# Kernel optimization log

Measured on AMD Instinct MI355X. Metric: run time of the kernel, lower is better.

Reference implementation:

```python
import jax, jax.numpy as jnp
import numpy as np

B, T, D, H, W = 256, 512, 64, 128, 256

def _init_linear(key, out_dim, in_dim):
    lim = 1.0 / np.sqrt(in_dim)
    return jax.random.uniform(key, (out_dim, in_dim), jnp.float32, -lim, lim)

def setup_inputs():
    key = jax.random.key(0)
    ks = jax.random.split(key, 12)
    inp = {}
    inp['ts'] = jnp.arange(T, dtype=jnp.float32)
    for n, k in zip(['coeffs_d', 'coeffs_c', 'coeffs_b', 'coeffs_a'], ks[:4]):
        inp[n] = jax.random.normal(k, (B, T - 1, D), jnp.float32) * 0.05
    # initial MLP: D -> W -> W -> H (relu hidden, identity final)
    inp['i_w0'] = _init_linear(ks[4], W, D); inp['i_b0'] = jnp.zeros((W,), jnp.float32)
    inp['i_w1'] = _init_linear(ks[5], W, W); inp['i_b1'] = jnp.zeros((W,), jnp.float32)
    inp['i_w2'] = _init_linear(ks[6], H, W); inp['i_b2'] = jnp.zeros((H,), jnp.float32)
    # func MLP: H -> W -> W -> H*D (softplus hidden, tanh final)
    inp['f_w0'] = _init_linear(ks[7], W, H); inp['f_b0'] = jnp.zeros((W,), jnp.float32)
    inp['f_w1'] = _init_linear(ks[8], W, W); inp['f_b1'] = jnp.zeros((W,), jnp.float32)
    inp['f_w2'] = _init_linear(ks[9], H * D, W); inp['f_b2'] = jnp.zeros((H * D,), jnp.float32)
    # readout linear: H -> 1
    inp['l_w'] = _init_linear(ks[10], 1, H); inp['l_b'] = jnp.zeros((1,), jnp.float32)
    return inp

def reference(ts, coeffs_d, coeffs_c, coeffs_b, coeffs_a,
              i_w0, i_b0, i_w1, i_b1, i_w2, i_b2,
              f_w0, f_b0, f_w1, f_b1, f_w2, f_b2,
              l_w, l_b):
    dt = ts[1] - ts[0]
    # cubic spline value at t=ts[0]: interval 0, frac 0 -> a[0]
    x0 = coeffs_a[:, 0, :]  # [B, D]
    h = jax.nn.relu(x0 @ i_w0.T + i_b0)
    h = jax.nn.relu(h @ i_w1.T + i_b1)
    y0 = h @ i_w2.T + i_b2  # [B, H]

    def step(carry, _):
        t, y = carry
        # cubic spline derivative at t: b + 2c*frac + 3d*frac^2 on interval idx
        idx = jnp.clip(jnp.searchsorted(ts, t, side='right') - 1, 0, T - 2)
        frac = t - ts[idx]
        deriv = coeffs_b[:, idx] + 2.0 * coeffs_c[:, idx] * frac + 3.0 * coeffs_d[:, idx] * (frac * frac)  # [B, D]
        # vector field f(y): [B, H, D]
        g = jax.nn.softplus(y @ f_w0.T + f_b0)
        g = jax.nn.softplus(g @ f_w1.T + f_b1)
        f = jnp.tanh(g @ f_w2.T + f_b2).reshape(B, H, D)
        # Euler step: y1 = y + (f @ dX/dt) * dt
        y1 = y + jnp.einsum('bhd,bd->bh', f, deriv) * dt
        return (t + dt, y1), y1

    _, ys = jax.lax.scan(step, (ts[0], y0), None, length=T)
    # prediction = sigmoid(linear(ys[-1]))[0], per batch element
    return jax.nn.sigmoid(ys[-1] @ l_w.T + l_b)[:, 0]  # [B]
```

## Files before the change

### kernel.cpp

```cpp
#include <hip/hip_runtime.h>
#include <hip/hip_bf16.h>
#include <stdint.h>


#define BB 256
#define DD 64
#define HH 128
#define WW 256
#define HD 8192
#define TSTEPS 512
#define PAD_Y 152
#define PAD_G 280

typedef __bf16 bf16x8 __attribute__((ext_vector_type(8)));
typedef __bf16 bf16x4 __attribute__((ext_vector_type(4)));
typedef float f32x4 __attribute__((ext_vector_type(4)));

__device__ __forceinline__ float softplus_f(float x) {
  return (x > 15.f) ? x : __logf(1.f + __expf(x));
}
__device__ __forceinline__ float tanh_f(float x) {
  float e = __expf(2.f * x);
  return 1.f - 2.f / (e + 1.f);
}
__device__ __forceinline__ float aloadf(const float* p) {
  return __hip_atomic_load(p, __ATOMIC_RELAXED, __HIP_MEMORY_SCOPE_AGENT);
}
__device__ __forceinline__ void astoref(float* p, float v) {
  __hip_atomic_store(p, v, __ATOMIC_RELAXED, __HIP_MEMORY_SCOPE_AGENT);
}
__device__ __forceinline__ uint32_t aloadu(const uint32_t* p) {
  return __hip_atomic_load(p, __ATOMIC_RELAXED, __HIP_MEMORY_SCOPE_AGENT);
}
__device__ __forceinline__ void astoreu(uint32_t* p, uint32_t v) {
  __hip_atomic_store(p, v, __ATOMIC_RELAXED, __HIP_MEMORY_SCOPE_AGENT);
}

__global__ void prep_kernel(const float* __restrict__ w0, const float* __restrict__ w1,
                            const float* __restrict__ w2,
                            __bf16* __restrict__ w0b, __bf16* __restrict__ w1b,
                            __bf16* __restrict__ w2b) {
  int stride = gridDim.x * blockDim.x;
  int i0 = blockIdx.x * blockDim.x + threadIdx.x;
  for (int i = i0; i < WW * HH; i += stride) w0b[i] = (__bf16)w0[i];
  for (int i = i0; i < WW * WW; i += stride) w1b[i] = (__bf16)w1[i];
  for (int i = i0; i < HD * WW; i += stride) w2b[i] = (__bf16)w2[i];
}

__global__ __launch_bounds__(256) void init_kernel(
    const float* __restrict__ ca, const float* __restrict__ iw0, const float* __restrict__ ib0,
    const float* __restrict__ iw1, const float* __restrict__ ib1,
    const float* __restrict__ iw2, const float* __restrict__ ib2,
    float* __restrict__ y0) {
  __shared__ float x0[DD];
  __shared__ float h0[WW];
  __shared__ float h1[WW];
  int b = blockIdx.x, t = threadIdx.x;
  if (t < DD) x0[t] = ca[((size_t)b * 511) * DD + t];
  __syncthreads();
  float a = ib0[t];
  for (int d = 0; d < DD; ++d) a = fmaf(x0[d], iw0[t * DD + d], a);
  h0[t] = fmaxf(a, 0.f);
  __syncthreads();
  a = ib1[t];
  for (int d = 0; d < WW; ++d) a = fmaf(h0[d], iw1[t * WW + d], a);
  h1[t] = fmaxf(a, 0.f);
  __syncthreads();
  if (t < HH) {
    a = ib2[t];
    for (int d = 0; d < WW; ++d) a = fmaf(h1[d], iw2[t * WW + d], a);
    y0[b * HH + t] = a;
  }
}

__global__ __launch_bounds__(512, 2) void step_persist(
    const __bf16* __restrict__ w0b, const __bf16* __restrict__ w1b, const __bf16* __restrict__ w2b,
    const float* __restrict__ fb0, const float* __restrict__ fb1, const float* __restrict__ fb2,
    const float* __restrict__ cbp, const float* __restrict__ ccp, const float* __restrict__ cdp,
    float* __restrict__ yA, float* __restrict__ pk, uint32_t* __restrict__ yflag)
{
  __shared__ __align__(16) __bf16 w2l[32768];
  __shared__ __align__(16) __bf16 yb[32 * PAD_Y];
  __shared__ __align__(16) __bf16 g0s[32 * PAD_G];
  __shared__ __align__(16) __bf16 g1s[32 * PAD_G];
  __shared__ float pbuf[8 * 32];

  const int tid = threadIdx.x;
  const int wv = tid >> 6;
  const int l = tid & 63;
  const int l16 = l & 15;
  const int lq = l >> 4;

  const int wid = blockIdx.x;
  const int grp = wid >> 5;
  const int j = wid & 31;
  const int rb = grp * 32;
  const int c0 = j * 256;

  for (int it = 0; it < 8; ++it) {
    int blk = tid + it * 512;
    int kq = blk >> 7, cl = blk & 127;
    int wv2 = cl >> 4, l16b = cl & 15;
    int kb = kq >> 2, lq2 = kq & 3;
    int col = c0 + wv2 * 32 + l16b;
    *(bf16x8*)&w2l[blk * 8] =
        *(const bf16x8*)&w2b[(size_t)col * WW + kb * 32 + lq2 * 8];
  }
  const int w2base = lq * 1024 + wv * 128 + l16 * 8;

  bf16x8 w0f[4][2], w1f[8][2], w2f1[8];
  #pragma unroll
  for (int c = 0; c < 2; ++c) {
    int col = wv * 32 + c * 16 + l16;
    #pragma unroll
    for (int kb = 0; kb < 4; ++kb)
      w0f[kb][c] = *(const bf16x8*)&w0b[col * HH + kb * 32 + lq * 8];
    #pragma unroll
    for (int kb = 0; kb < 8; ++kb)
      w1f[kb][c] = *(const bf16x8*)&w1b[col * WW + kb * 32 + lq * 8];
  }
  {
    int col = c0 + wv * 32 + 16 + l16;
    #pragma unroll
    for (int kb = 0; kb < 8; ++kb)
      w2f1[kb] = *(const bf16x8*)&w2b[(size_t)col * WW + kb * 32 + lq * 8];
  }
  f32x4 b0r[2], b1r[2], b2r[2];
  #pragma unroll
  for (int c = 0; c < 2; ++c) {
    b0r[c] = *(const f32x4*)&fb0[wv * 32 + c * 16 + lq * 4];
    b1r[c] = *(const f32x4*)&fb1[wv * 32 + c * 16 + lq * 4];
    b2r[c] = *(const f32x4*)&fb2[c0 + wv * 32 + c * 16 + lq * 4];
  }

  size_t cb2[2];
  #pragma unroll
  for (int bt = 0; bt < 2; ++bt)
    cb2[bt] = ((size_t)(rb + bt * 16 + l16) * 511) * DD + (wv & 1) * 32 + lq * 4;

  float yreg = 0.f;
  int myidx = 0;
  if (tid < 128) {
    int r = tid & 31, hl = tid >> 5;
    myidx = (rb + r) * HH + (4 * j + hl);
    yreg = yA[myidx];
    astoref(&pk[myidx], yreg);
  }
  __syncthreads();
  if (tid == 0) astoreu(&yflag[grp * 32 + j], 1u);

  const int ps = tid & 31;
  const int pw = tid >> 5;
  const uint32_t* myflag = &yflag[grp * 32 + ps];

  for (int k = 0; k < TSTEPS; ++k) {
    const uint32_t want = (uint32_t)(k + 1);
    const float* src = pk + (size_t)(k & 1) * (BB * HH);
    float* dst = pk + (size_t)((k + 1) & 1) * (BB * HH);

    f32x4 dvv[2][2];
    {
      size_t ko = (size_t)((k <= 510) ? k : 510) * DD;
      #pragma unroll
      for (int bt = 0; bt < 2; ++bt)
        #pragma unroll
        for (int c = 0; c < 2; ++c) {
          size_t off = cb2[bt] + ko + c * 16;
          dvv[bt][c] = *(const f32x4*)&cbp[off];
          if (k == 511) {
            f32x4 cc = *(const f32x4*)&ccp[off];
            f32x4 dd = *(const f32x4*)&cdp[off];
            #pragma unroll
            for (int r = 0; r < 4; ++r)
              dvv[bt][c][r] += 2.f * cc[r] + 3.f * dd[r];
          }
        }
    }

    {
      int spins = 0;
      while (aloadu(myflag) < want) {
        __builtin_amdgcn_s_sleep(1);
        if (++spins > (1 << 20)) break;
      }
      __asm__ __volatile__("" ::: "memory");
      #pragma unroll
      for (int r2 = 0; r2 < 2; ++r2) {
        int row = 2 * pw + r2;
        const float* ysrc = &src[(rb + row) * HH + 4 * ps];
        bf16x4 o;
        #pragma unroll
        for (int q = 0; q < 4; ++q) o[q] = (__bf16)aloadf(&ysrc[q]);
        *(bf16x4*)&yb[row * PAD_Y + 4 * ps] = o;
      }
    }
    __syncthreads();

    {
      f32x4 acc[2][2];
      #pragma unroll
      for (int c = 0; c < 2; ++c) { acc[c][0] = b0r[c]; acc[c][1] = b0r[c]; }
      #pragma unroll
      for (int kb = 0; kb < 4; ++kb) {
        bf16x8 y0 = *(const bf16x8*)&yb[l16 * PAD_Y + kb * 32 + lq * 8];
        bf16x8 y1 = *(const bf16x8*)&yb[(16 + l16) * PAD_Y + kb * 32 + lq * 8];
        #pragma unroll
        for (int c = 0; c < 2; ++c) {
          acc[c][0] = __builtin_amdgcn_mfma_f32_16x16x32_bf16(w0f[kb][c], y0, acc[c][0], 0, 0, 0);
          acc[c][1] = __builtin_amdgcn_mfma_f32_16x16x32_bf16(w0f[kb][c], y1, acc[c][1], 0, 0, 0);
        }
      }
      #pragma unroll
      for (int c = 0; c < 2; ++c)
        #pragma unroll
        for (int bt = 0; bt < 2; ++bt) {
          bf16x4 o;
          #pragma unroll
          for (int r = 0; r < 4; ++r)
            o[r] = (__bf16)softplus_f(acc[c][bt][r]);
          *(bf16x4*)&g0s[(bt * 16 + l16) * PAD_G + wv * 32 + c * 16 + lq * 4] = o;
        }
    }
    __syncthreads();

    {
      f32x4 acc[2][2];
      #pragma unroll
      for (int c = 0; c < 2; ++c) { acc[c][0] = b1r[c]; acc[c][1] = b1r[c]; }
      #pragma unroll
      for (int kb = 0; kb < 8; ++kb) {
        bf16x8 a0 = *(const bf16x8*)&g0s[l16 * PAD_G + kb * 32 + lq * 8];
        bf16x8 a1 = *(const bf16x8*)&g0s[(16 + l16) * PAD_G + kb * 32 + lq * 8];
        #pragma unroll
        for (int c = 0; c < 2; ++c) {
          acc[c][0] = __builtin_amdgcn_mfma_f32_16x16x32_bf16(w1f[kb][c], a0, acc[c][0], 0, 0, 0);
          acc[c][1] = __builtin_amdgcn_mfma_f32_16x16x32_bf16(w1f[kb][c], a1, acc[c][1], 0, 0, 0);
        }
      }
      #pragma unroll
      for (int c = 0; c < 2; ++c)
        #pragma unroll
        for (int bt = 0; bt < 2; ++bt) {
          bf16x4 o;
          #pragma unroll
          for (int r = 0; r < 4; ++r)
            o[r] = (__bf16)softplus_f(acc[c][bt][r]);
          *(bf16x4*)&g1s[(bt * 16 + l16) * PAD_G + wv * 32 + c * 16 + lq * 4] = o;
        }
    }
    __syncthreads();

    {
      f32x4 acc[2][2];
      #pragma unroll
      for (int c = 0; c < 2; ++c) { acc[c][0] = b2r[c]; acc[c][1] = b2r[c]; }
      #pragma unroll
      for (int kb = 0; kb < 8; ++kb) {
        bf16x8 a0 = *(const bf16x8*)&g1s[l16 * PAD_G + kb * 32 + lq * 8];
        bf16x8 a1 = *(const bf16x8*)&g1s[(16 + l16) * PAD_G + kb * 32 + lq * 8];
        bf16x8 wf0 = *(const bf16x8*)&w2l[w2base + kb * 4096];
        acc[0][0] = __builtin_amdgcn_mfma_f32_16x16x32_bf16(wf0, a0, acc[0][0], 0, 0, 0);
        acc[0][1] = __builtin_amdgcn_mfma_f32_16x16x32_bf16(wf0, a1, acc[0][1], 0, 0, 0);
        acc[1][0] = __builtin_amdgcn_mfma_f32_16x16x32_bf16(w2f1[kb], a0, acc[1][0], 0, 0, 0);
        acc[1][1] = __builtin_amdgcn_mfma_f32_16x16x32_bf16(w2f1[kb], a1, acc[1][1], 0, 0, 0);
      }
      #pragma unroll
      for (int bt = 0; bt < 2; ++bt) {
        float p = 0.f;
        #pragma unroll
        for (int c = 0; c < 2; ++c) {
          #pragma unroll
          for (int r = 0; r < 4; ++r) {
            float f = tanh_f(acc[c][bt][r]);
            p = fmaf(f, dvv[bt][c][r], p);
          }
        }
        p += __shfl_xor(p, 16);
        p += __shfl_xor(p, 32);
        if (l < 16) pbuf[wv * 32 + bt * 16 + l] = p;
      }
    }
    __syncthreads();

    if (tid < 128) {
      int hl = tid >> 5, r = tid & 31;
      yreg += pbuf[(2 * hl) * 32 + r] + pbuf[(2 * hl + 1) * 32 + r];
      astoref(&dst[myidx], yreg);
    }
    __syncthreads();
    if (tid == 0) astoreu(&yflag[grp * 32 + j], (uint32_t)(k + 2));
  }

  if (tid < 128) yA[myidx] = yreg;
}

__global__ __launch_bounds__(256) void final_kernel(const float* __restrict__ y,
                                                    const float* __restrict__ lw,
                                                    const float* __restrict__ lb,
                                                    float* __restrict__ out) {
  int b = threadIdx.x;
  float a = lb[0];
  for (int h = 0; h < HH; ++h) a = fmaf(y[b * HH + h], lw[h], a);
  out[b] = 1.f / (1.f + __expf(-a));
}

extern "C" void kernel_launch(void* const* d_in, const int* in_sizes, int n_in,
                              void* d_out, int out_size, void* d_ws, size_t ws_size,
                              hipStream_t stream) {
  const float* cdp = (const float*)d_in[1];
  const float* ccp = (const float*)d_in[2];
  const float* cbp = (const float*)d_in[3];
  const float* cap = (const float*)d_in[4];
  const float* iw0 = (const float*)d_in[5];
  const float* ib0 = (const float*)d_in[6];
  const float* iw1 = (const float*)d_in[7];
  const float* ib1 = (const float*)d_in[8];
  const float* iw2 = (const float*)d_in[9];
  const float* ib2 = (const float*)d_in[10];
  const float* fw0 = (const float*)d_in[11];
  const float* fb0 = (const float*)d_in[12];
  const float* fw1 = (const float*)d_in[13];
  const float* fb1 = (const float*)d_in[14];
  const float* fw2 = (const float*)d_in[15];
  const float* fb2 = (const float*)d_in[16];
  const float* lw  = (const float*)d_in[17];
  const float* lb  = (const float*)d_in[18];

  char* ws = (char*)d_ws;
  __bf16* w0b = (__bf16*)(ws);
  __bf16* w1b = (__bf16*)(ws + 65536);
  __bf16* w2b = (__bf16*)(ws + 196608);
  float* yA = (float*)(ws + 4390912);
  float* pk = (float*)(ws + 4521984);
  uint32_t* yflag = (uint32_t*)(ws + 4784128);

  hipMemsetAsync(yflag, 0, 1024, stream);
  prep_kernel<<<512, 256, 0, stream>>>(fw0, fw1, fw2, w0b, w1b, w2b);
  init_kernel<<<BB, 256, 0, stream>>>(cap, iw0, ib0, iw1, ib1, iw2, ib2, yA);
  step_persist<<<256, 512, 0, stream>>>(w0b, w1b, w2b, fb0, fb1, fb2,
                                        cbp, ccp, cdp, yA, pk, yflag);
  final_kernel<<<1, 256, 0, stream>>>(yA, lw, lb, (float*)d_out);

  (void)in_sizes; (void)n_in; (void)out_size; (void)ws_size;
}
```

Baseline: 3.681 ms.

## Remap W2 stage so each wave owns whole h outputs, signal per-wave

The third GEMM stage now assigns each wave 16 batch rows by 64 output columns (one full h index across D), so the D-reduction finishes inside a wave via shuffles. This removes the LDS partial-sum buffer and two block-wide barriers per step. Each wave publishes its y slice and increments the group flag with an atomic add, and consumers wait for eight increments. The cost is more weight registers per wave and that correctness now rests on the vmcnt wait ordering the y stores ahead of the relaxed flag increment.

```diff
diff --git a/kernel.cpp b/kernel.cpp
--- a/kernel.cpp
+++ b/kernel.cpp
@@ -31,9 +31,6 @@
 }
 __device__ __forceinline__ uint32_t aloadu(const uint32_t* p) {
   return __hip_atomic_load(p, __ATOMIC_RELAXED, __HIP_MEMORY_SCOPE_AGENT);
-}
-__device__ __forceinline__ void astoreu(uint32_t* p, uint32_t v) {
-  __hip_atomic_store(p, v, __ATOMIC_RELAXED, __HIP_MEMORY_SCOPE_AGENT);
 }
 
 __global__ void prep_kernel(const float* __restrict__ w0, const float* __restrict__ w1,
@@ -83,7 +80,6 @@
   __shared__ __align__(16) __bf16 yb[32 * PAD_Y];
   __shared__ __align__(16) __bf16 g0s[32 * PAD_G];
   __shared__ __align__(16) __bf16 g1s[32 * PAD_G];
-  __shared__ float pbuf[8 * 32];
 
   const int tid = threadIdx.x;
   const int wv = tid >> 6;
@@ -96,19 +92,20 @@
   const int j = wid & 31;
   const int rb = grp * 32;
   const int c0 = j * 256;
+  const int rt = wv >> 2;
+  const int hq = wv & 3;
 
   for (int it = 0; it < 8; ++it) {
     int blk = tid + it * 512;
     int kq = blk >> 7, cl = blk & 127;
-    int wv2 = cl >> 4, l16b = cl & 15;
     int kb = kq >> 2, lq2 = kq & 3;
-    int col = c0 + wv2 * 32 + l16b;
+    int col = c0 + (cl >> 5) * 64 + (cl & 31);
     *(bf16x8*)&w2l[blk * 8] =
         *(const bf16x8*)&w2b[(size_t)col * WW + kb * 32 + lq2 * 8];
   }
-  const int w2base = lq * 1024 + wv * 128 + l16 * 8;
-
-  bf16x8 w0f[4][2], w1f[8][2], w2f1[8];
+  const int w2base = lq * 1024 + (hq * 32 + l16) * 8;
+
+  bf16x8 w0f[4][2], w1f[8][2], w2f[8][2];
   #pragma unroll
   for (int c = 0; c < 2; ++c) {
     int col = wv * 32 + c * 16 + l16;
@@ -118,63 +115,56 @@
     #pragma unroll
     for (int kb = 0; kb < 8; ++kb)
       w1f[kb][c] = *(const bf16x8*)&w1b[col * WW + kb * 32 + lq * 8];
-  }
-  {
-    int col = c0 + wv * 32 + 16 + l16;
+    int colC = c0 + hq * 64 + 32 + c * 16 + l16;
     #pragma unroll
     for (int kb = 0; kb < 8; ++kb)
-      w2f1[kb] = *(const bf16x8*)&w2b[(size_t)col * WW + kb * 32 + lq * 8];
-  }
-  f32x4 b0r[2], b1r[2], b2r[2];
+      w2f[kb][c] = *(const bf16x8*)&w2b[(size_t)colC * WW + kb * 32 + lq * 8];
+  }
+  f32x4 b0r[2], b1r[2], b2r[4];
   #pragma unroll
   for (int c = 0; c < 2; ++c) {
     b0r[c] = *(const f32x4*)&fb0[wv * 32 + c * 16 + lq * 4];
     b1r[c] = *(const f32x4*)&fb1[wv * 32 + c * 16 + lq * 4];
-    b2r[c] = *(const f32x4*)&fb2[c0 + wv * 32 + c * 16 + lq * 4];
-  }
-
-  size_t cb2[2];
+  }
   #pragma unroll
-  for (int bt = 0; bt < 2; ++bt)
-    cb2[bt] = ((size_t)(rb + bt * 16 + l16) * 511) * DD + (wv & 1) * 32 + lq * 4;
-
+  for (int c = 0; c < 4; ++c)
+    b2r[c] = *(const f32x4*)&fb2[c0 + hq * 64 + c * 16 + lq * 4];
+
+  const size_t dvbase = ((size_t)(rb + rt * 16 + l16) * 511) * DD + lq * 4;
+
+  const int myidx = (rb + rt * 16 + l16) * HH + (4 * j + hq);
+  uint32_t* const flg = &yflag[grp * 32 + j];
   float yreg = 0.f;
-  int myidx = 0;
-  if (tid < 128) {
-    int r = tid & 31, hl = tid >> 5;
-    myidx = (rb + r) * HH + (4 * j + hl);
+  if (l < 16) {
     yreg = yA[myidx];
     astoref(&pk[myidx], yreg);
   }
-  __syncthreads();
-  if (tid == 0) astoreu(&yflag[grp * 32 + j], 1u);
+  __asm__ __volatile__("s_waitcnt vmcnt(0)" ::: "memory");
+  if (l == 0) __hip_atomic_fetch_add(flg, 1u, __ATOMIC_RELAXED, __HIP_MEMORY_SCOPE_AGENT);
 
   const int ps = tid & 31;
   const int pw = tid >> 5;
   const uint32_t* myflag = &yflag[grp * 32 + ps];
 
   for (int k = 0; k < TSTEPS; ++k) {
-    const uint32_t want = (uint32_t)(k + 1);
+    const uint32_t want = 8u * (uint32_t)(k + 1);
     const float* src = pk + (size_t)(k & 1) * (BB * HH);
     float* dst = pk + (size_t)((k + 1) & 1) * (BB * HH);
 
-    f32x4 dvv[2][2];
-    {
-      size_t ko = (size_t)((k <= 510) ? k : 510) * DD;
-      #pragma unroll
-      for (int bt = 0; bt < 2; ++bt)
-        #pragma unroll
-        for (int c = 0; c < 2; ++c) {
-          size_t off = cb2[bt] + ko + c * 16;
-          dvv[bt][c] = *(const f32x4*)&cbp[off];
-          if (k == 511) {
-            f32x4 cc = *(const f32x4*)&ccp[off];
-            f32x4 dd = *(const f32x4*)&cdp[off];
-            #pragma unroll
-            for (int r = 0; r < 4; ++r)
-              dvv[bt][c][r] += 2.f * cc[r] + 3.f * dd[r];
-          }
-        }
+    f32x4 dvv[4];
+    {
+      size_t ko = dvbase + (size_t)((k <= 510) ? k : 510) * DD;
+      #pragma unroll
+      for (int c = 0; c < 4; ++c) dvv[c] = *(const f32x4*)&cbp[ko + c * 16];
+      if (k == 511) {
+        #pragma unroll
+        for (int c = 0; c < 4; ++c) {
+          f32x4 cc = *(const f32x4*)&ccp[ko + c * 16];
+          f32x4 dd = *(const f32x4*)&cdp[ko + c * 16];
+          #pragma unroll
+          for (int r = 0; r < 4; ++r) dvv[c][r] += 2.f * cc[r] + 3.f * dd[r];
+        }
+      }
     }
 
     {
@@ -251,47 +241,37 @@
     __syncthreads();
 
     {
-      f32x4 acc[2][2];
-      #pragma unroll
-      for (int c = 0; c < 2; ++c) { acc[c][0] = b2r[c]; acc[c][1] = b2r[c]; }
+      f32x4 acc[4] = {b2r[0], b2r[1], b2r[2], b2r[3]};
       #pragma unroll
       for (int kb = 0; kb < 8; ++kb) {
-        bf16x8 a0 = *(const bf16x8*)&g1s[l16 * PAD_G + kb * 32 + lq * 8];
-        bf16x8 a1 = *(const bf16x8*)&g1s[(16 + l16) * PAD_G + kb * 32 + lq * 8];
-        bf16x8 wf0 = *(const bf16x8*)&w2l[w2base + kb * 4096];
-        acc[0][0] = __builtin_amdgcn_mfma_f32_16x16x32_bf16(wf0, a0, acc[0][0], 0, 0, 0);
-        acc[0][1] = __builtin_amdgcn_mfma_f32_16x16x32_bf16(wf0, a1, acc[0][1], 0, 0, 0);
-        acc[1][0] = __builtin_amdgcn_mfma_f32_16x16x32_bf16(w2f1[kb], a0, acc[1][0], 0, 0, 0);
-        acc[1][1] = __builtin_amdgcn_mfma_f32_16x16x32_bf16(w2f1[kb], a1, acc[1][1], 0, 0, 0);
-      }
-      #pragma unroll
-      for (int bt = 0; bt < 2; ++bt) {
-        float p = 0.f;
-        #pragma unroll
-        for (int c = 0; c < 2; ++c) {
-          #pragma unroll
-          for (int r = 0; r < 4; ++r) {
-            float f = tanh_f(acc[c][bt][r]);
-            p = fmaf(f, dvv[bt][c][r], p);
-          }
-        }
-        p += __shfl_xor(p, 16);
-        p += __shfl_xor(p, 32);
-        if (l < 16) pbuf[wv * 32 + bt * 16 + l] = p;
-      }
-    }
-    __syncthreads();
-
-    if (tid < 128) {
-      int hl = tid >> 5, r = tid & 31;
-      yreg += pbuf[(2 * hl) * 32 + r] + pbuf[(2 * hl + 1) * 32 + r];
-      astoref(&dst[myidx], yreg);
-    }
-    __syncthreads();
-    if (tid == 0) astoreu(&yflag[grp * 32 + j], (uint32_t)(k + 2));
-  }
-
-  if (tid < 128) yA[myidx] = yreg;
+        bf16x8 a0 = *(const bf16x8*)&g1s[(rt * 16 + l16) * PAD_G + kb * 32 + lq * 8];
+        bf16x8 wl0 = *(const bf16x8*)&w2l[w2base + kb * 4096];
+        bf16x8 wl1 = *(const bf16x8*)&w2l[w2base + kb * 4096 + 128];
+        acc[0] = __builtin_amdgcn_mfma_f32_16x16x32_bf16(wl0, a0, acc[0], 0, 0, 0);
+        acc[1] = __builtin_amdgcn_mfma_f32_16x16x32_bf16(wl1, a0, acc[1], 0, 0, 0);
+        acc[2] = __builtin_amdgcn_mfma_f32_16x16x32_bf16(w2f[kb][0], a0, acc[2], 0, 0, 0);
+        acc[3] = __builtin_amdgcn_mfma_f32_16x16x32_bf16(w2f[kb][1], a0, acc[3], 0, 0, 0);
+      }
+      float pp = 0.f;
+      #pragma unroll
+      for (int c = 0; c < 4; ++c)
+        #pragma unroll
+        for (int r = 0; r < 4; ++r) {
+          float f = tanh_f(acc[c][r]);
+          pp = fmaf(f, dvv[c][r], pp);
+        }
+      pp += __shfl_xor(pp, 16);
+      pp += __shfl_xor(pp, 32);
+      if (l < 16) {
+        yreg += pp;
+        astoref(&dst[myidx], yreg);
+      }
+    }
+    __asm__ __volatile__("s_waitcnt vmcnt(0)" ::: "memory");
+    if (l == 0) __hip_atomic_fetch_add(flg, 1u, __ATOMIC_RELAXED, __HIP_MEMORY_SCOPE_AGENT);
+  }
+
+  if (l < 16) yA[myidx] = yreg;
 }
 
 __global__ __launch_bounds__(256) void final_kernel(const float* __restrict__ y,
```

Result: slower. 8.369 ms (+127.3%).
